# Performance work log

Measured on AMD Instinct MI355X. Metric: run time of the kernel, lower is better.

Reference implementation:

```python
import jax, jax.numpy as jnp
import numpy as np

B, N, H, K = 256, 1024, 256, 5
NEG_SLOPE = 0.01  # torch LeakyReLU default


def setup_inputs() -> dict:
    key = jax.random.key(0)
    k1, k2, k3, k4 = jax.random.split(key, 4)
    h = jax.random.normal(k1, (B, N, H), dtype=jnp.float32)
    n_nodes = jax.random.randint(k2, (B,), 0, N)
    attention_query = jax.random.normal(k3, (B, H), dtype=jnp.float32)
    W = jax.random.normal(k4, (1, 2 * H), dtype=jnp.float32) * (1.0 / np.sqrt(2 * H))
    return {"h": h, "n_nodes": n_nodes, "attention_query": attention_query, "W": W}


def reference(h, n_nodes, attention_query, W):
    # --- DGL SortPooling ---
    # 1) sort each node's feature vector in ascending order along channels
    feat = jnp.sort(h, axis=-1)                                  # [B, N, H]
    # 2) rank nodes by last sorted channel (max feature); mask padded nodes
    sort_key = feat[..., -1]                                     # [B, N]
    node_mask = jnp.arange(N)[None, :] < n_nodes[:, None]        # [B, N]
    sort_key = jnp.where(node_mask, sort_key, -jnp.inf)
    top_vals, top_idx = jax.lax.top_k(sort_key, K)               # [B, K]
    sel = jnp.take_along_axis(feat, top_idx[..., None], axis=1)  # [B, K, H]
    # 3) zero-pad graphs with fewer than K nodes
    valid = jnp.isfinite(top_vals)[..., None]                    # [B, K, 1]
    output = jnp.where(valid, sel, 0.0)                          # [B, K, H]
    # --- attention-weighted sum ---
    q = jnp.broadcast_to(attention_query[:, None, :], (B, K, H))
    cat = jnp.concatenate([output, q], axis=-1)                  # [B, K, 2H]
    logits = jax.nn.leaky_relu(jnp.einsum('bkf,of->bko', cat, W), NEG_SLOPE)
    atten = jax.nn.softmax(logits, axis=1)                       # [B, K, 1]
    return jnp.sum(output * atten, axis=1)                       # [B, H]
```

## Files before the change

### kernel.cpp

```cpp
#include <hip/hip_runtime.h>
#include <hip/hip_bf16.h>
#include <math.h>

#define BGRAPHS 256
#define NNODES  1024
#define HDIM    256
#define KSEL    5
#define NEG_SLOPE 0.01f

#define NPB    128
#define UNROLL 4

__global__ __launch_bounds__(256) void node_max_kernel(
        const float* __restrict__ h,
        const int* __restrict__ n_nodes,
        float* __restrict__ keys) {
    __shared__ float keys_s[NPB];
    const int t    = threadIdx.x;
    const int wave = t >> 6;
    const int lane = t & 63;

    const long long base = (long long)blockIdx.x * NPB;
    const int b   = (int)(base >> 10);
    const int nb0 = (int)(base & 1023);
    int nv = n_nodes[b] - nb0;
    nv = nv < 0 ? 0 : (nv > NPB ? NPB : nv);

    if (t < NPB) keys_s[t] = -INFINITY;
    __syncthreads();

    const float4* __restrict__ h4 = (const float4*)h;
    const long long idx = (base + wave) * 64 + lane;

    const int niter = (nv + 3) >> 2;
    for (int ii = 0; ii < niter; ii += UNROLL) {
        float4 d[UNROLL];
        bool   act[UNROLL];
#pragma unroll
        for (int u = 0; u < UNROLL; ++u) {
            int local = (ii + u) * 4 + wave;
            act[u] = (local < nv) && (ii + u < niter);
            if (act[u])
                d[u] = h4[idx + (long long)(ii + u) * 4 * 64];
        }
#pragma unroll
        for (int u = 0; u < UNROLL; ++u) {
            if (act[u]) {
                float m = fmaxf(fmaxf(d[u].x, d[u].y), fmaxf(d[u].z, d[u].w));
#pragma unroll
                for (int off = 32; off > 0; off >>= 1)
                    m = fmaxf(m, __shfl_xor(m, off, 64));
                if (lane == 0)
                    keys_s[(ii + u) * 4 + wave] = m;
            }
        }
    }
    __syncthreads();
    if (t < NPB)
        keys[base + t] = keys_s[t];
}

__global__ __launch_bounds__(256) void topk_attn_kernel(
        const float* __restrict__ h,
        const float* __restrict__ q,
        const float* __restrict__ W,
        const float* __restrict__ keys,
        float* __restrict__ out) {
    __shared__ float keys_s[NNODES];
    __shared__ float red_v[256];
    __shared__ int   red_i[256];
    __shared__ float sorted_s[KSEL][HDIM];
    __shared__ float vals_s[HDIM];
    __shared__ float dots[KSEL];
    __shared__ float atten[KSEL];
    __shared__ float cb_s;
    __shared__ int   top_idx[KSEL];
    __shared__ float top_val[KSEL];

    const int t = threadIdx.x;
    const int b = blockIdx.x;

#pragma unroll
    for (int i = 0; i < 4; ++i)
        keys_s[t + 256 * i] = keys[b * NNODES + t + 256 * i];

    red_v[t] = q[b * HDIM + t] * W[HDIM + t];
    __syncthreads();
    for (int s = 128; s > 0; s >>= 1) {
        if (t < s) red_v[t] += red_v[t + s];
        __syncthreads();
    }
    if (t == 0) cb_s = red_v[0];
    __syncthreads();

    for (int k = 0; k < KSEL; ++k) {
        float bv = -INFINITY;
        int   bi = 0x7fffffff;
#pragma unroll
        for (int i = 0; i < 4; ++i) {
            int j = t * 4 + i;
            float v = keys_s[j];
            if (v > bv || (v == bv && j < bi)) { bv = v; bi = j; }
        }
        red_v[t] = bv;
        red_i[t] = bi;
        __syncthreads();
        for (int s = 128; s > 0; s >>= 1) {
            if (t < s) {
                float ov = red_v[t + s];
                int   oi = red_i[t + s];
                if (ov > red_v[t] || (ov == red_v[t] && oi < red_i[t])) {
                    red_v[t] = ov;
                    red_i[t] = oi;
                }
            }
            __syncthreads();
        }
        if (t == 0) {
            top_idx[k] = red_i[0];
            top_val[k] = red_v[0];
            keys_s[red_i[0]] = -INFINITY;
        }
        __syncthreads();
    }

    for (int k = 0; k < KSEL; ++k) {
        int  sel   = top_idx[k];
        bool valid = (top_val[k] != -INFINITY);
        float v = 0.0f;
        if (valid)
            v = h[((long long)b * NNODES + sel) * HDIM + t];
        vals_s[t] = v;
        __syncthreads();
        int rank = 0;
        for (int j = 0; j < HDIM; ++j) {
            float vj = vals_s[j];
            rank += (vj < v) || (vj == v && j < t);
        }
        sorted_s[k][rank] = v;
        __syncthreads();
    }

    float w1 = W[t];
    for (int k = 0; k < KSEL; ++k) {
        red_v[t] = sorted_s[k][t] * w1;
        __syncthreads();
        for (int s = 128; s > 0; s >>= 1) {
            if (t < s) red_v[t] += red_v[t + s];
            __syncthreads();
        }
        if (t == 0) dots[k] = red_v[0];
        __syncthreads();
    }

    if (t == 0) {
        float lg[KSEL];
        float mx = -INFINITY;
#pragma unroll
        for (int k = 0; k < KSEL; ++k) {
            float x = dots[k] + cb_s;
            lg[k] = (x > 0.0f) ? x : NEG_SLOPE * x;
            mx = fmaxf(mx, lg[k]);
        }
        float den = 0.0f;
#pragma unroll
        for (int k = 0; k < KSEL; ++k) { lg[k] = expf(lg[k] - mx); den += lg[k]; }
#pragma unroll
        for (int k = 0; k < KSEL; ++k) atten[k] = lg[k] / den;
    }
    __syncthreads();

    float o = 0.0f;
#pragma unroll
    for (int k = 0; k < KSEL; ++k)
        o += atten[k] * sorted_s[k][t];

    out[b * HDIM + t] = o;
}

extern "C" void kernel_launch(void* const* d_in, const int* in_sizes, int n_in,
                              void* d_out, int out_size, void* d_ws, size_t ws_size,
                              hipStream_t stream) {
    const float* h  = (const float*)d_in[0];
    const int*   nn = (const int*)d_in[1];
    const float* q  = (const float*)d_in[2];
    const float* W  = (const float*)d_in[3];
    float*       out = (float*)d_out;

    float* keys = (float*)d_ws;

    node_max_kernel<<<(BGRAPHS * NNODES) / NPB, 256, 0, stream>>>(h, nn, keys);
    topk_attn_kernel<<<BGRAPHS, 256, 0, stream>>>(h, q, W, keys, out);
}
```

Measured before the change: 376.5 us.

## Rewrite top-k attention with packed-key wave reductions and swizzle node-max block order

The top-k selection now packs order-preserving float keys with inverted indices into 64-bit values and reduces them with wave shuffles and a 4-entry cross-wave step, replacing the shared-memory tree reductions and their many barriers. All five selected rows are loaded and ranked in a single pass using float4 LDS reads. The dot products and the softmax are also computed with shuffles and redundantly in every thread. Separately, the node-max kernel remaps block IDs with a multiplicative permutation to spread uneven per-graph work across CUs. The rewrite depends on the ordf encoding and the 997 permutation being bijective over the 2048 blocks.

Result: faster. 368.9 us (-2.0%).

```diff
diff --git a/kernel.cpp b/kernel.cpp
--- a/kernel.cpp
+++ b/kernel.cpp
@@ -1,5 +1,4 @@
 #include <hip/hip_runtime.h>
-#include <hip/hip_bf16.h>
 #include <math.h>
 
 #define BGRAPHS 256
@@ -10,6 +9,11 @@
 
 #define NPB    128
 #define UNROLL 4
+
+__device__ __forceinline__ unsigned int ordf(float f) {
+    unsigned int u = __float_as_uint(f);
+    return (u & 0x80000000u) ? ~u : (u | 0x80000000u);
+}
 
 __global__ __launch_bounds__(256) void node_max_kernel(
         const float* __restrict__ h,
@@ -20,7 +24,8 @@
     const int wave = t >> 6;
     const int lane = t & 63;
 
-    const long long base = (long long)blockIdx.x * NPB;
+    const int cid = (int)((blockIdx.x * 997u) & 2047u);
+    const long long base = (long long)cid * NPB;
     const int b   = (int)(base >> 10);
     const int nb0 = (int)(base & 1023);
     int nv = n_nodes[b] - nb0;
@@ -66,114 +71,136 @@
         const float* __restrict__ W,
         const float* __restrict__ keys,
         float* __restrict__ out) {
-    __shared__ float keys_s[NNODES];
-    __shared__ float red_v[256];
-    __shared__ int   red_i[256];
-    __shared__ float sorted_s[KSEL][HDIM];
-    __shared__ float vals_s[HDIM];
-    __shared__ float dots[KSEL];
-    __shared__ float atten[KSEL];
-    __shared__ float cb_s;
-    __shared__ int   top_idx[KSEL];
-    __shared__ float top_val[KSEL];
-
-    const int t = threadIdx.x;
-    const int b = blockIdx.x;
-
-#pragma unroll
-    for (int i = 0; i < 4; ++i)
-        keys_s[t + 256 * i] = keys[b * NNODES + t + 256 * i];
-
-    red_v[t] = q[b * HDIM + t] * W[HDIM + t];
-    __syncthreads();
-    for (int s = 128; s > 0; s >>= 1) {
-        if (t < s) red_v[t] += red_v[t + s];
+    __shared__ float cb_red[4];
+    __shared__ unsigned long long wmax[KSEL][4];
+    __shared__ __align__(16) float row_s[KSEL][HDIM];
+    __shared__ __align__(16) float sorted_s[KSEL][HDIM];
+    __shared__ float dred[4][KSEL];
+
+    const int t    = threadIdx.x;
+    const int lane = t & 63;
+    const int wave = t >> 6;
+    const int b    = blockIdx.x;
+
+    const float4 kv = ((const float4*)(keys + b * NNODES))[t];
+    const float qv = q[b * HDIM + t];
+    const float w1 = W[t];
+    const float w2 = W[HDIM + t];
+
+    unsigned long long pk0 = ((unsigned long long)ordf(kv.x) << 32) | (unsigned int)(1023 - (4 * t + 0));
+    unsigned long long pk1 = ((unsigned long long)ordf(kv.y) << 32) | (unsigned int)(1023 - (4 * t + 1));
+    unsigned long long pk2 = ((unsigned long long)ordf(kv.z) << 32) | (unsigned int)(1023 - (4 * t + 2));
+    unsigned long long pk3 = ((unsigned long long)ordf(kv.w) << 32) | (unsigned int)(1023 - (4 * t + 3));
+
+    float c = qv * w2;
+#pragma unroll
+    for (int off = 32; off > 0; off >>= 1)
+        c += __shfl_xor(c, off, 64);
+    if (lane == 0) cb_red[wave] = c;
+
+    const unsigned int ORD_NINF = 0x007FFFFFu;
+    int widx[KSEL];
+    int wvalid[KSEL];
+#pragma unroll
+    for (int k = 0; k < KSEL; ++k) {
+        unsigned long long p = pk0;
+        p = pk1 > p ? pk1 : p;
+        p = pk2 > p ? pk2 : p;
+        p = pk3 > p ? pk3 : p;
+#pragma unroll
+        for (int off = 32; off > 0; off >>= 1) {
+            unsigned long long o = __shfl_xor(p, off, 64);
+            p = o > p ? o : p;
+        }
+        if (lane == 0) wmax[k][wave] = p;
         __syncthreads();
-    }
-    if (t == 0) cb_s = red_v[0];
-    __syncthreads();
-
-    for (int k = 0; k < KSEL; ++k) {
-        float bv = -INFINITY;
-        int   bi = 0x7fffffff;
-#pragma unroll
-        for (int i = 0; i < 4; ++i) {
-            int j = t * 4 + i;
-            float v = keys_s[j];
-            if (v > bv || (v == bv && j < bi)) { bv = v; bi = j; }
-        }
-        red_v[t] = bv;
-        red_i[t] = bi;
-        __syncthreads();
-        for (int s = 128; s > 0; s >>= 1) {
-            if (t < s) {
-                float ov = red_v[t + s];
-                int   oi = red_i[t + s];
-                if (ov > red_v[t] || (ov == red_v[t] && oi < red_i[t])) {
-                    red_v[t] = ov;
-                    red_i[t] = oi;
-                }
-            }
-            __syncthreads();
-        }
-        if (t == 0) {
-            top_idx[k] = red_i[0];
-            top_val[k] = red_v[0];
-            keys_s[red_i[0]] = -INFINITY;
-        }
-        __syncthreads();
-    }
-
-    for (int k = 0; k < KSEL; ++k) {
-        int  sel   = top_idx[k];
-        bool valid = (top_val[k] != -INFINITY);
+        unsigned long long p0 = wmax[k][0], p1 = wmax[k][1];
+        unsigned long long p2 = wmax[k][2], p3 = wmax[k][3];
+        p = p0 > p1 ? p0 : p1;
+        unsigned long long pq = p2 > p3 ? p2 : p3;
+        p = pq > p ? pq : p;
+
+        const int idx = 1023 - (int)(unsigned int)(p & 0xFFFFFFFFull);
+        widx[k]   = idx;
+        wvalid[k] = ((unsigned int)(p >> 32)) != ORD_NINF;
+
+        const bool own = (idx >> 2) == t;
+        const int  s   = idx & 3;
+        pk0 = (own && s == 0) ? 0ull : pk0;
+        pk1 = (own && s == 1) ? 0ull : pk1;
+        pk2 = (own && s == 2) ? 0ull : pk2;
+        pk3 = (own && s == 3) ? 0ull : pk3;
+    }
+
+    float vk[KSEL];
+#pragma unroll
+    for (int k = 0; k < KSEL; ++k) {
         float v = 0.0f;
-        if (valid)
-            v = h[((long long)b * NNODES + sel) * HDIM + t];
-        vals_s[t] = v;
-        __syncthreads();
-        int rank = 0;
-        for (int j = 0; j < HDIM; ++j) {
-            float vj = vals_s[j];
-            rank += (vj < v) || (vj == v && j < t);
-        }
-        sorted_s[k][rank] = v;
-        __syncthreads();
-    }
-
-    float w1 = W[t];
-    for (int k = 0; k < KSEL; ++k) {
-        red_v[t] = sorted_s[k][t] * w1;
-        __syncthreads();
-        for (int s = 128; s > 0; s >>= 1) {
-            if (t < s) red_v[t] += red_v[t + s];
-            __syncthreads();
-        }
-        if (t == 0) dots[k] = red_v[0];
-        __syncthreads();
-    }
-
-    if (t == 0) {
-        float lg[KSEL];
-        float mx = -INFINITY;
+        if (wvalid[k])
+            v = h[((long long)b * NNODES + widx[k]) * HDIM + t];
+        vk[k] = v;
+    }
+#pragma unroll
+    for (int k = 0; k < KSEL; ++k)
+        row_s[k][t] = vk[k];
+    __syncthreads();
+
+    int rk[KSEL] = {0, 0, 0, 0, 0};
+    const float4* r4 = (const float4*)&row_s[0][0];
+#pragma unroll 4
+    for (int jj = 0; jj < HDIM / 4; ++jj) {
+        const int j = jj * 4;
 #pragma unroll
         for (int k = 0; k < KSEL; ++k) {
-            float x = dots[k] + cb_s;
-            lg[k] = (x > 0.0f) ? x : NEG_SLOPE * x;
-            mx = fmaxf(mx, lg[k]);
-        }
-        float den = 0.0f;
-#pragma unroll
-        for (int k = 0; k < KSEL; ++k) { lg[k] = expf(lg[k] - mx); den += lg[k]; }
-#pragma unroll
-        for (int k = 0; k < KSEL; ++k) atten[k] = lg[k] / den;
-    }
-    __syncthreads();
+            float4 a = r4[k * (HDIM / 4) + jj];
+            rk[k] += (int)((a.x < vk[k]) | ((a.x == vk[k]) & (j     < t)));
+            rk[k] += (int)((a.y < vk[k]) | ((a.y == vk[k]) & (j + 1 < t)));
+            rk[k] += (int)((a.z < vk[k]) | ((a.z == vk[k]) & (j + 2 < t)));
+            rk[k] += (int)((a.w < vk[k]) | ((a.w == vk[k]) & (j + 3 < t)));
+        }
+    }
+#pragma unroll
+    for (int k = 0; k < KSEL; ++k)
+        sorted_s[k][rk[k]] = vk[k];
+    __syncthreads();
+
+    float sv[KSEL], d[KSEL];
+#pragma unroll
+    for (int k = 0; k < KSEL; ++k) {
+        sv[k] = sorted_s[k][t];
+        d[k]  = sv[k] * w1;
+    }
+#pragma unroll
+    for (int off = 32; off > 0; off >>= 1) {
+#pragma unroll
+        for (int k = 0; k < KSEL; ++k)
+            d[k] += __shfl_xor(d[k], off, 64);
+    }
+    if (lane == 0) {
+#pragma unroll
+        for (int k = 0; k < KSEL; ++k)
+            dred[wave][k] = d[k];
+    }
+    __syncthreads();
+
+    const float cb = cb_red[0] + cb_red[1] + cb_red[2] + cb_red[3];
+    float lg[KSEL];
+    float mx = -INFINITY;
+#pragma unroll
+    for (int k = 0; k < KSEL; ++k) {
+        float x = dred[0][k] + dred[1][k] + dred[2][k] + dred[3][k] + cb;
+        lg[k] = (x > 0.0f) ? x : NEG_SLOPE * x;
+        mx = fmaxf(mx, lg[k]);
+    }
+    float den = 0.0f;
+#pragma unroll
+    for (int k = 0; k < KSEL; ++k) { lg[k] = expf(lg[k] - mx); den += lg[k]; }
+    const float inv_den = 1.0f / den;
 
     float o = 0.0f;
 #pragma unroll
     for (int k = 0; k < KSEL; ++k)
-        o += atten[k] * sorted_s[k][t];
+        o += (lg[k] * inv_den) * sv[k];
 
     out[b * HDIM + t] = o;
 }
```
